# Kernel tuning notes

Hardware: AMD Instinct MI355X
Metric: run time of the kernel (lower is better)

The kernel has to match this reference:

```python
import jax, jax.numpy as jnp
import numpy as np

B, C_FEAT, H_F, W_F = 16, 256, 80, 80
C_ILL, K, H_Z, W_Z = 64, 3, 40, 40


def setup_inputs() -> dict:
    key = jax.random.key(0)
    k1, k2, k3, k4, k5, k6, k7 = jax.random.split(key, 7)
    feat = jax.random.normal(k1, (B, C_FEAT, H_F, W_F), dtype=jnp.float32)
    Z = jax.random.normal(k2, (B, C_ILL, H_Z, W_Z), dtype=jnp.float32)
    P = jax.random.uniform(k3, (B, K, H_Z, W_Z), dtype=jnp.float32)
    # Expert 1x1-conv params (original zero-inits; use small random for nontrivial math)
    Wg = jax.random.normal(k4, (K, C_FEAT, C_ILL), dtype=jnp.float32) * 0.02
    bg = jax.random.normal(k5, (K, C_FEAT), dtype=jnp.float32) * 0.02
    Wb = jax.random.normal(k6, (K, C_FEAT, C_ILL), dtype=jnp.float32) * 0.02
    bb = jax.random.normal(k7, (K, C_FEAT), dtype=jnp.float32) * 0.02
    return {"feat": feat, "Z": Z, "P": P, "Wg": Wg, "bg": bg, "Wb": Wb, "bb": bb}


def reference(feat, Z, P, Wg, bg, Wb, bb):
    Bb, C, H, W = feat.shape
    # bilinear upsample, half-pixel centers (== torch align_corners=False)
    Z_up = jax.image.resize(Z, (Z.shape[0], Z.shape[1], H, W), method='bilinear')
    P_up = jax.image.resize(P, (P.shape[0], P.shape[1], H, W), method='bilinear')
    # router-weighted illumination features: [B,K,D,H,W]
    ZP = jnp.einsum('bkhw,bdhw->bkdhw', P_up, Z_up)
    # soft-routed 1x1-conv experts, fused across K (weights + router-weighted biases)
    delta_gamma = jnp.einsum('bkdhw,kcd->bchw', ZP, Wg) + jnp.einsum('bkhw,kc->bchw', P_up, bg)
    delta_beta = jnp.einsum('bkdhw,kcd->bchw', ZP, Wb) + jnp.einsum('bkhw,kc->bchw', P_up, bb)
    # FiLM residual modulation
    return feat * (1.0 + delta_gamma) + delta_beta
```

## Files before the change

kernel.cpp:

```cpp
#include <hip/hip_runtime.h>
#include <hip/hip_bf16.h>

#define NB   16
#define NC   256
#define HF   80
#define WF   80
#define NPIX 6400
#define ND   64
#define NK   3
#define NKC  7
#define NPB  400
#define A_G_STRIDE  (NKC * 4 * 512)


typedef __bf16 bf16;
typedef __bf16 bf16x8 __attribute__((ext_vector_type(8)));
typedef float  floatx4 __attribute__((ext_vector_type(4)));

__global__ __launch_bounds__(256) void pack_A_kernel(
    const float* __restrict__ Wg, const float* __restrict__ bg,
    const float* __restrict__ Wb, const float* __restrict__ bb,
    bf16* __restrict__ A2)
{
    int i = blockIdx.x * 256 + threadIdx.x;
    int lane = i & 63;
    int j2 = i >> 6;
    int mt = j2 & 3;
    int j3 = j2 >> 2;
    int kc = j3 % 7;
    int g  = j3 / 7;
    int l15 = lane & 15, q = lane >> 4;
    int cbase = (g >> 1) * 64 + (g & 1) * 32;
    int c = cbase + (mt & 1) * 16 + l15;
    const float* W    = (mt >= 2) ? Wb : Wg;
    const float* bias = (mt >= 2) ? bb : bg;
    int kd0 = kc * 32 + q * 8;

    bf16x8 v;
    if (kd0 < NK * ND) {
        int k = kd0 >> 6, d = kd0 & 63;
        const float* src = W + ((size_t)k * NC + c) * ND + d;
        #pragma unroll
        for (int j = 0; j < 8; ++j) v[j] = (bf16)src[j];
    } else if (kd0 == NK * ND) {
        #pragma unroll
        for (int j = 0; j < 8; ++j) v[j] = (bf16)0.0f;
        v[0] = (bf16)bias[0 * NC + c];
        v[1] = (bf16)bias[1 * NC + c];
        v[2] = (bf16)bias[2 * NC + c];
    } else {
        #pragma unroll
        for (int j = 0; j < 8; ++j) v[j] = (bf16)0.0f;
    }
    *reinterpret_cast<bf16x8*>(A2 + (size_t)i * 8) = v;
}

__global__ __launch_bounds__(256) void build_z_kernel(
    const float* __restrict__ Z, const float* __restrict__ P,
    float* __restrict__ ZF, float* __restrict__ PU)
{
    __shared__ float z_up[WF][ND + 1];
    __shared__ float p_up[WF][NK];

    const int bid = blockIdx.x;
    const int b   = bid / HF;
    const int h   = bid - b * HF;
    const int t   = threadIdx.x;

    float srch = 0.5f * (float)h - 0.25f;
    float flh  = floorf(srch);
    float fh   = srch - flh;
    int h0 = (int)flh, h1 = h0 + 1;
    h0 = max(h0, 0); h1 = min(h1, 40 - 1);

    #pragma unroll 4
    for (int i = 0; i < 20; ++i) {
        int e = t + 256 * i;
        int d = e / WF;
        int w = e - d * WF;
        float srcw = 0.5f * (float)w - 0.25f;
        float flw  = floorf(srcw);
        float fw   = srcw - flw;
        int w0 = (int)flw, w1 = w0 + 1;
        w0 = max(w0, 0); w1 = min(w1, 40 - 1);
        const float* Zr = Z + (size_t)(b * ND + d) * (40 * 40);
        float z00 = Zr[h0 * 40 + w0], z01 = Zr[h0 * 40 + w1];
        float z10 = Zr[h1 * 40 + w0], z11 = Zr[h1 * 40 + w1];
        float zi0 = z00 + fw * (z01 - z00);
        float zi1 = z10 + fw * (z11 - z10);
        z_up[w][d] = zi0 + fh * (zi1 - zi0);
    }
    if (t < WF * NK) {
        int w = t / NK;
        int k = t - w * NK;
        float srcw = 0.5f * (float)w - 0.25f;
        float flw  = floorf(srcw);
        float fw   = srcw - flw;
        int w0 = (int)flw, w1 = w0 + 1;
        w0 = max(w0, 0); w1 = min(w1, 40 - 1);
        const float* Pr = P + (size_t)(b * NK + k) * (40 * 40);
        float p00 = Pr[h0 * 40 + w0], p01 = Pr[h0 * 40 + w1];
        float p10 = Pr[h1 * 40 + w0], p11 = Pr[h1 * 40 + w1];
        float pi0 = p00 + fw * (p01 - p00);
        float pi1 = p10 + fw * (p11 - p10);
        p_up[w][k] = pi0 + fh * (pi1 - pi0);
    }
    __syncthreads();

    for (int i = t; i < 640; i += 256) {
        int lane = i & 63;
        int j2   = i >> 6;
        int half = j2 & 1;
        int pb_l = j2 >> 1;
        int l15 = lane & 15, q = lane >> 4;
        int w   = pb_l * 16 + l15;
        int d0  = half * 32 + q * 8;
        float* dst = ZF + ((((size_t)(b * NPB + h * 5 + pb_l)) * 2 + half) * 64 + lane) * 8;
        floatx4 v0, v1;
        #pragma unroll
        for (int j = 0; j < 4; ++j) { v0[j] = z_up[w][d0 + j]; v1[j] = z_up[w][d0 + 4 + j]; }
        *reinterpret_cast<floatx4*>(dst)     = v0;
        *reinterpret_cast<floatx4*>(dst + 4) = v1;
    }
    if (t < 240) {
        int pb_l = t / 48;
        int rem  = t - pb_l * 48;
        int k    = rem >> 4;
        int l15  = rem & 15;
        PU[(((size_t)(b * NPB + h * 5 + pb_l)) * 3 + k) * 16 + l15] = p_up[pb_l * 16 + l15][k];
    }
}

__global__ __launch_bounds__(256, 2) void gemm_film_kernel(
    const bf16* __restrict__ A2, const float* __restrict__ ZF,
    const float* __restrict__ PU,
    const float* __restrict__ feat, float* __restrict__ out)
{
    const int ntb = blockIdx.x;
    const int ct  = blockIdx.y;
    const int b   = blockIdx.z;
    const int tid  = threadIdx.x;
    const int lane = tid & 63;
    const int wv   = tid >> 6;
    const int mq   = wv & 1;
    const int nh   = wv >> 1;
    const int l15  = lane & 15;
    const int q    = lane >> 4;

    const int g     = ct * 2 + mq;
    const int cbase = ct * 64 + mq * 32;
    const int pb0   = ntb * 8 + nh * 4;
    const int pix0  = pb0 * 16;

    floatx4 zf[4][2][2];
    #pragma unroll
    for (int nt = 0; nt < 4; ++nt)
        #pragma unroll
        for (int hf = 0; hf < 2; ++hf) {
            const float* cp = ZF + ((((size_t)(b * NPB + pb0 + nt)) * 2 + hf) * 64 + lane) * 8;
            zf[nt][hf][0] = *reinterpret_cast<const floatx4*>(cp);
            zf[nt][hf][1] = *reinterpret_cast<const floatx4*>(cp + 4);
        }
    float pv[4][3];
    #pragma unroll
    for (int nt = 0; nt < 4; ++nt)
        #pragma unroll
        for (int k = 0; k < 3; ++k)
            pv[nt][k] = PU[(((size_t)(b * NPB + pb0 + nt)) * 3 + k) * 16 + l15];

    const bf16* aptr = A2 + (size_t)g * A_G_STRIDE + (size_t)lane * 8;
    bf16x8 aA[4], aB[4];
    #pragma unroll
    for (int mt = 0; mt < 4; ++mt)
        aA[mt] = *reinterpret_cast<const bf16x8*>(aptr + mt * 512);
    #pragma unroll
    for (int mt = 0; mt < 4; ++mt)
        aB[mt] = *reinterpret_cast<const bf16x8*>(aptr + 2048 + mt * 512);

    floatx4 acc[4][4] = {};

    #pragma unroll
    for (int kc = 0; kc < NKC; ++kc) {
        bf16x8 bfr[4];
        if (kc < 6) {
            const int hf = kc & 1;
            const int k  = kc >> 1;
            #pragma unroll
            for (int nt = 0; nt < 4; ++nt) {
                float p = pv[nt][k];
                #pragma unroll
                for (int j = 0; j < 4; ++j) {
                    bfr[nt][j]     = (bf16)(p * zf[nt][hf][0][j]);
                    bfr[nt][j + 4] = (bf16)(p * zf[nt][hf][1][j]);
                }
            }
        } else {
            #pragma unroll
            for (int nt = 0; nt < 4; ++nt) {
                #pragma unroll
                for (int j = 0; j < 8; ++j) bfr[nt][j] = (bf16)0.0f;
                if (q == 0) {
                    bfr[nt][0] = (bf16)pv[nt][0];
                    bfr[nt][1] = (bf16)pv[nt][1];
                    bfr[nt][2] = (bf16)pv[nt][2];
                }
            }
        }
        #pragma unroll
        for (int mt = 0; mt < 4; ++mt)
            #pragma unroll
            for (int nt = 0; nt < 4; ++nt)
                acc[mt][nt] = __builtin_amdgcn_mfma_f32_16x16x32_bf16(
                    aA[mt], bfr[nt], acc[mt][nt], 0, 0, 0);
        #pragma unroll
        for (int mt = 0; mt < 4; ++mt) aA[mt] = aB[mt];
        if (kc + 2 < NKC) {
            #pragma unroll
            for (int mt = 0; mt < 4; ++mt)
                aB[mt] = *reinterpret_cast<const bf16x8*>(aptr + (kc + 2) * 2048 + mt * 512);
        }
    }

    const float* featb = feat + (size_t)b * NC * NPIX;
    float* outb = out + (size_t)b * NC * NPIX;
    #pragma unroll
    for (int mt = 0; mt < 2; ++mt) {
        #pragma unroll
        for (int r = 0; r < 4; ++r) {
            int c = cbase + mt * 16 + q * 4 + r;
            const float* frow = featb + (size_t)c * NPIX;
            float* orow = outb + (size_t)c * NPIX;
            #pragma unroll
            for (int nt = 0; nt < 4; ++nt) {
                int pix = pix0 + nt * 16 + l15;
                float gaccum = acc[mt][nt][r];
                float be     = acc[mt + 2][nt][r];
                float f      = frow[pix];
                orow[pix] = f * (1.0f + gaccum) + be;
            }
        }
    }
}

extern "C" void kernel_launch(void* const* d_in, const int* in_sizes, int n_in,
                              void* d_out, int out_size, void* d_ws, size_t ws_size,
                              hipStream_t stream)
{
    (void)in_sizes; (void)n_in; (void)out_size; (void)ws_size;
    const float* feat = (const float*)d_in[0];
    const float* Z    = (const float*)d_in[1];
    const float* P    = (const float*)d_in[2];
    const float* Wg   = (const float*)d_in[3];
    const float* bg   = (const float*)d_in[4];
    const float* Wb   = (const float*)d_in[5];
    const float* bb   = (const float*)d_in[6];

    float* ZF = (float*)d_ws;
    float* PU = ZF + (size_t)NB * NPB * 2 * 64 * 8;
    bf16*  Apk = (bf16*)(PU + (size_t)NB * NPB * 3 * 16);
    float* out = (float*)d_out;

    pack_A_kernel<<<56, 256, 0, stream>>>(Wg, bg, Wb, bb, Apk);
    build_z_kernel<<<NB * HF, 256, 0, stream>>>(Z, P, ZF, PU);

    dim3 grid(NPIX / 128, NC / 64, NB);
    gemm_film_kernel<<<grid, 256, 0, stream>>>(Apk, ZF, PU, feat, out);
}
```

Measured before the change: 241.5 us.

## Swap MFMA operands for vectorized FiLM epilogue, prefetch feat, merge prep kernels

Swapping the A and B operands of the MFMA makes each lane hold four consecutive pixels for a single channel. The epilogue can then use 16-byte float4 loads of feat and stores of out instead of scalar strided accesses. The feat tile is loaded before the GEMM loop so its latency overlaps the MFMA work, which costs extra registers. The weight-packing and upsample-building kernels are merged into one launch to remove one kernel launch.

```diff
diff --git a/kernel.cpp b/kernel.cpp
--- a/kernel.cpp
+++ b/kernel.cpp
@@ -17,55 +17,55 @@
 typedef __bf16 bf16x8 __attribute__((ext_vector_type(8)));
 typedef float  floatx4 __attribute__((ext_vector_type(4)));
 
-__global__ __launch_bounds__(256) void pack_A_kernel(
+__global__ __launch_bounds__(256) void prep_kernel(
+    const float* __restrict__ Z, const float* __restrict__ P,
     const float* __restrict__ Wg, const float* __restrict__ bg,
     const float* __restrict__ Wb, const float* __restrict__ bb,
-    bf16* __restrict__ A2)
-{
-    int i = blockIdx.x * 256 + threadIdx.x;
-    int lane = i & 63;
-    int j2 = i >> 6;
-    int mt = j2 & 3;
-    int j3 = j2 >> 2;
-    int kc = j3 % 7;
-    int g  = j3 / 7;
-    int l15 = lane & 15, q = lane >> 4;
-    int cbase = (g >> 1) * 64 + (g & 1) * 32;
-    int c = cbase + (mt & 1) * 16 + l15;
-    const float* W    = (mt >= 2) ? Wb : Wg;
-    const float* bias = (mt >= 2) ? bb : bg;
-    int kd0 = kc * 32 + q * 8;
-
-    bf16x8 v;
-    if (kd0 < NK * ND) {
-        int k = kd0 >> 6, d = kd0 & 63;
-        const float* src = W + ((size_t)k * NC + c) * ND + d;
-        #pragma unroll
-        for (int j = 0; j < 8; ++j) v[j] = (bf16)src[j];
-    } else if (kd0 == NK * ND) {
-        #pragma unroll
-        for (int j = 0; j < 8; ++j) v[j] = (bf16)0.0f;
-        v[0] = (bf16)bias[0 * NC + c];
-        v[1] = (bf16)bias[1 * NC + c];
-        v[2] = (bf16)bias[2 * NC + c];
-    } else {
-        #pragma unroll
-        for (int j = 0; j < 8; ++j) v[j] = (bf16)0.0f;
-    }
-    *reinterpret_cast<bf16x8*>(A2 + (size_t)i * 8) = v;
-}
-
-__global__ __launch_bounds__(256) void build_z_kernel(
-    const float* __restrict__ Z, const float* __restrict__ P,
-    float* __restrict__ ZF, float* __restrict__ PU)
+    float* __restrict__ ZF, float* __restrict__ PU, bf16* __restrict__ A2)
 {
     __shared__ float z_up[WF][ND + 1];
     __shared__ float p_up[WF][NK];
 
     const int bid = blockIdx.x;
+    const int t   = threadIdx.x;
+
+    if (bid >= NB * HF) {
+        int i = (bid - NB * HF) * 256 + t;
+        int lane = i & 63;
+        int j2 = i >> 6;
+        int mt = j2 & 3;
+        int j3 = j2 >> 2;
+        int kc = j3 % 7;
+        int g  = j3 / 7;
+        int l15 = lane & 15, q = lane >> 4;
+        int cbase = (g >> 1) * 64 + (g & 1) * 32;
+        int c = cbase + (mt & 1) * 16 + l15;
+        const float* W    = (mt >= 2) ? Wb : Wg;
+        const float* bias = (mt >= 2) ? bb : bg;
+        int kd0 = kc * 32 + q * 8;
+
+        bf16x8 v;
+        if (kd0 < NK * ND) {
+            int k = kd0 >> 6, d = kd0 & 63;
+            const float* src = W + ((size_t)k * NC + c) * ND + d;
+            #pragma unroll
+            for (int j = 0; j < 8; ++j) v[j] = (bf16)src[j];
+        } else if (kd0 == NK * ND) {
+            #pragma unroll
+            for (int j = 0; j < 8; ++j) v[j] = (bf16)0.0f;
+            v[0] = (bf16)bias[0 * NC + c];
+            v[1] = (bf16)bias[1 * NC + c];
+            v[2] = (bf16)bias[2 * NC + c];
+        } else {
+            #pragma unroll
+            for (int j = 0; j < 8; ++j) v[j] = (bf16)0.0f;
+        }
+        *reinterpret_cast<bf16x8*>(A2 + (size_t)i * 8) = v;
+        return;
+    }
+
     const int b   = bid / HF;
     const int h   = bid - b * HF;
-    const int t   = threadIdx.x;
 
     float srch = 0.5f * (float)h - 0.25f;
     float flh  = floorf(srch);
@@ -177,6 +177,15 @@
     for (int mt = 0; mt < 4; ++mt)
         aB[mt] = *reinterpret_cast<const bf16x8*>(aptr + 2048 + mt * 512);
 
+    const float* featb = feat + ((size_t)(b * NC + cbase + l15)) * NPIX + pix0 + q * 4;
+    floatx4 fv[2][4];
+    #pragma unroll
+    for (int mt = 0; mt < 2; ++mt)
+        #pragma unroll
+        for (int nt = 0; nt < 4; ++nt)
+            fv[mt][nt] = *reinterpret_cast<const floatx4*>(
+                featb + (size_t)mt * 16 * NPIX + nt * 16);
+
     floatx4 acc[4][4] = {};
 
     #pragma unroll
@@ -211,7 +220,7 @@
             #pragma unroll
             for (int nt = 0; nt < 4; ++nt)
                 acc[mt][nt] = __builtin_amdgcn_mfma_f32_16x16x32_bf16(
-                    aA[mt], bfr[nt], acc[mt][nt], 0, 0, 0);
+                    bfr[nt], aA[mt], acc[mt][nt], 0, 0, 0);
         #pragma unroll
         for (int mt = 0; mt < 4; ++mt) aA[mt] = aB[mt];
         if (kc + 2 < NKC) {
@@ -221,23 +230,19 @@
         }
     }
 
-    const float* featb = feat + (size_t)b * NC * NPIX;
-    float* outb = out + (size_t)b * NC * NPIX;
+    float* outb = out + ((size_t)(b * NC + cbase + l15)) * NPIX + pix0 + q * 4;
     #pragma unroll
     for (int mt = 0; mt < 2; ++mt) {
         #pragma unroll
-        for (int r = 0; r < 4; ++r) {
-            int c = cbase + mt * 16 + q * 4 + r;
-            const float* frow = featb + (size_t)c * NPIX;
-            float* orow = outb + (size_t)c * NPIX;
-            #pragma unroll
-            for (int nt = 0; nt < 4; ++nt) {
-                int pix = pix0 + nt * 16 + l15;
-                float gaccum = acc[mt][nt][r];
-                float be     = acc[mt + 2][nt][r];
-                float f      = frow[pix];
-                orow[pix] = f * (1.0f + gaccum) + be;
-            }
+        for (int nt = 0; nt < 4; ++nt) {
+            floatx4 f  = fv[mt][nt];
+            floatx4 ga = acc[mt][nt];
+            floatx4 be = acc[mt + 2][nt];
+            floatx4 o;
+            #pragma unroll
+            for (int j = 0; j < 4; ++j)
+                o[j] = f[j] * (1.0f + ga[j]) + be[j];
+            *reinterpret_cast<floatx4*>(outb + (size_t)mt * 16 * NPIX + nt * 16) = o;
         }
     }
 }
@@ -260,8 +265,7 @@
     bf16*  Apk = (bf16*)(PU + (size_t)NB * NPB * 3 * 16);
     float* out = (float*)d_out;
 
-    pack_A_kernel<<<56, 256, 0, stream>>>(Wg, bg, Wb, bb, Apk);
-    build_z_kernel<<<NB * HF, 256, 0, stream>>>(Z, P, ZF, PU);
+    prep_kernel<<<NB * HF + 56, 256, 0, stream>>>(Z, P, Wg, bg, Wb, bb, ZF, PU, Apk);
 
     dim3 grid(NPIX / 128, NC / 64, NB);
     gemm_film_kernel<<<grid, 256, 0, stream>>>(Apk, ZF, PU, feat, out);
```

After: 241.3 us. About the same (-0.1%).
